# Optimization experiments

Hardware: AMD Instinct MI355X
Metric: run time of the kernel (lower is better)

## Reference

```python
import jax, jax.numpy as jnp
import numpy as np

B, N, C = 2, 65536, 256
HEADS, DIM_HEAD, SLICE_NUM = 8, 64, 64
INNER = HEADS * DIM_HEAD


def setup_inputs() -> dict:
    key = jax.random.key(0)
    ks = jax.random.split(key, 7)
    s_in = 1.0 / np.sqrt(C)
    s_dh = 1.0 / np.sqrt(DIM_HEAD)
    return {
        "x": jax.random.normal(ks[0], (B, N, C), dtype=jnp.float32),
        "Wx": jax.random.uniform(ks[1], (C, INNER), jnp.float32, -s_in, s_in),
        "bx": jax.random.uniform(ks[2], (INNER,), jnp.float32, -s_in, s_in),
        "Wfx": jax.random.uniform(ks[3], (C, INNER), jnp.float32, -s_in, s_in),
        "bfx": jax.random.uniform(ks[4], (INNER,), jnp.float32, -s_in, s_in),
        "Wslice": jax.random.uniform(ks[5], (DIM_HEAD, SLICE_NUM), jnp.float32, -s_dh, s_dh),
        "bslice": jax.random.uniform(ks[6], (SLICE_NUM,), jnp.float32, -s_dh, s_dh),
        "temperature": jnp.ones((1, HEADS, 1, 1), dtype=jnp.float32) * 0.5,
    }


def reference(x, Wx, bx, Wfx, bfx, Wslice, bslice, temperature):
    b, n, _ = x.shape
    # Linear projections, split heads: (B, N, H*D) -> (B, H, N, D)
    px = (x @ Wx + bx).reshape(b, n, HEADS, DIM_HEAD).transpose(0, 2, 1, 3)
    fx = (x @ Wfx + bfx).reshape(b, n, HEADS, DIM_HEAD).transpose(0, 2, 1, 3)
    # Project onto slices: (B, H, N, S)
    slice_proj = px @ Wslice + bslice
    # Temperature-scaled softmax over slices
    temp = jnp.clip(temperature, 0.5, 5.0)
    slice_weights = jax.nn.softmax(slice_proj / temp, axis=-1)
    # Normalize by per-slice mass over tokens, then aggregate
    slice_norm = slice_weights.sum(axis=2)  # (B, H, S)
    normed = slice_weights / (slice_norm[:, :, None, :] + 0.01)
    slice_tokens = jnp.einsum("bhns,bhnd->bhsd", normed, fx)
    return slice_tokens
```

## Files before the change

kernel.cpp:

```cpp
#include <hip/hip_runtime.h>
#include <hip/hip_bf16.h>


typedef __attribute__((ext_vector_type(8))) short short8;
typedef __attribute__((ext_vector_type(4))) short short4v;
typedef __attribute__((ext_vector_type(4))) float float4v;
typedef __attribute__((ext_vector_type(2))) unsigned int uint2v;

#define WPITCH 264
#define MP 36

__device__ __forceinline__ unsigned short f2bf(float f) {
    union { float f; unsigned int u; } v; v.f = f;
    unsigned int r = (v.u + 0x7FFFu + ((v.u >> 16) & 1u)) >> 16;
    return (unsigned short)r;
}

__device__ __forceinline__ unsigned int pack2(float a, float b) {
    __hip_bfloat162 h = __float22bfloat162_rn(float2{a, b});
    union { __hip_bfloat162 h; unsigned int u; } cv; cv.h = h;
    return cv.u;
}

__global__ __launch_bounds__(256)
void msfe_xprep(const float* __restrict__ x, unsigned short* __restrict__ xf) {
    __shared__ unsigned short Xs[64 * WPITCH];
    const int blk = blockIdx.x;
    const int tid = threadIdx.x;
    const float4v* xg = (const float4v*)(x + (long)blk * 64 * 256);
    #pragma unroll
    for (int i = 0; i < 16; ++i) {
        float4v v = xg[tid + i * 256];
        int f = (tid + i * 256) * 4;
        int row = f >> 8, col = f & 255;
        unsigned int lo = pack2(v.x, v.y), hi = pack2(v.z, v.w);
        *(unsigned int*)(Xs + row * WPITCH + col)     = lo;
        *(unsigned int*)(Xs + row * WPITCH + col + 2) = hi;
    }
    __syncthreads();
    const int wv = tid >> 6, lane = tid & 63;
    const int quad = lane >> 4, l16 = lane & 15;
    const int chunkL = wv >> 1, tw = wv & 1;
    unsigned short* ob = xf + (((long)(blk * 2 + chunkL) * 2 + tw) * 4096) + (long)lane * 8;
    const int row0 = chunkL * 32 + tw * 16 + l16;
    #pragma unroll
    for (int ks = 0; ks < 8; ++ks) {
        short8 o = *(const short8*)(Xs + row0 * WPITCH + ks * 32 + quad * 8);
        *(short8*)(ob + ks * 512) = o;
    }
}

__global__ __launch_bounds__(256)
void msfe_prep4(const float* __restrict__ Wx, const float* __restrict__ bx,
                const float* __restrict__ Wfx,
                const float* __restrict__ Wslice, const float* __restrict__ bslice,
                unsigned short* __restrict__ WtF, float* __restrict__ bcv) {
    const int b = blockIdx.x, t = threadIdx.x;
    if (b < 256) {
        const int head = b >> 5, oct = b & 31;
        __shared__ float Wsl[64 * 65];
        __shared__ float WxS[8 * 64];
        __shared__ unsigned short stg[8 * 64];
        #pragma unroll
        for (int i = 0; i < 16; ++i) {
            int idx = i * 256 + t; int d = idx >> 6, s = idx & 63;
            Wsl[d * 65 + s] = Wslice[idx];
        }
        #pragma unroll
        for (int i = 0; i < 2; ++i) {
            int idx = i * 256 + t; int j = idx >> 6, d = idx & 63;
            WxS[j * 64 + d] = Wx[(long)(oct * 8 + j) * 512 + head * 64 + d];
        }
        __syncthreads();
        const int s = t & 63;
        #pragma unroll
        for (int rep = 0; rep < 2; ++rep) {
            int j = (t >> 6) + rep * 4;
            float a0 = 0.f, a1 = 0.f, a2 = 0.f, a3 = 0.f;
            #pragma unroll
            for (int d = 0; d < 64; d += 4) {
                a0 += WxS[j * 64 + d]     * Wsl[(d)     * 65 + s];
                a1 += WxS[j * 64 + d + 1] * Wsl[(d + 1) * 65 + s];
                a2 += WxS[j * 64 + d + 2] * Wsl[(d + 2) * 65 + s];
                a3 += WxS[j * 64 + d + 3] * Wsl[(d + 3) * 65 + s];
            }
            stg[j * 64 + s] = f2bf((a0 + a1) + (a2 + a3));
        }
        __syncthreads();
        if (t < 64) {
            int nt = t >> 4, l16 = t & 15;
            int ks = oct >> 2, quad = oct & 3;
            int lane = quad * 16 + l16;
            short8 o;
            #pragma unroll
            for (int j = 0; j < 8; ++j) o[j] = (short)stg[j * 64 + nt * 16 + l16];
            *(short8*)(WtF + ((((long)(0 * 8 + head) * 4 + nt) * 8 + ks) * 64 + lane) * 8) = o;
        }
    } else if (b < 320) {
        const int head = (b - 256) >> 3, ks = (b - 256) & 7;
        const int nt = t >> 6, lane = t & 63;
        const int quad = lane >> 4, l16 = lane & 15;
        short8 o;
        #pragma unroll
        for (int j = 0; j < 8; ++j)
            o[j] = (short)f2bf(Wfx[(long)(ks * 32 + quad * 8 + j) * 512 + head * 64 + nt * 16 + l16]);
        *(short8*)(WtF + ((((long)(1 * 8 + head) * 4 + nt) * 8 + ks) * 64 + lane) * 8) = o;
    } else {
        #pragma unroll
        for (int p = 0; p < 2; ++p) {
            int j = t + p * 256;
            int h = j >> 6, s = j & 63;
            float bsum = bslice[s];
            for (int d = 0; d < 64; ++d) bsum += bx[h * 64 + d] * Wslice[d * 64 + s];
            bcv[j] = bsum;
        }
    }
}

__global__ __launch_bounds__(256, 2)
void msfe_main5(const unsigned short* __restrict__ xf,
                const unsigned short* __restrict__ WtF,
                const float* __restrict__ bcv,
                const float* __restrict__ bfx,
                const float* __restrict__ temperature,
                float* __restrict__ Tg, float* __restrict__ ng) {
    __shared__ unsigned short wT[2][64 * MP];
    __shared__ unsigned short fT[2][64 * MP];

    const int tid  = threadIdx.x;
    const int lane = tid & 63;
    const int wv   = tid >> 6;
    const int quad = lane >> 4;
    const int l16  = lane & 15;

    const int bidx = blockIdx.x;
    const int tile = (bidx >> 6) * 8 + (bidx & 7);
    const int head = (bidx >> 3) & 7;
    const int batch = tile >> 7;

    const int proj = wv >> 1;
    const int tw   = wv & 1;

    short8 wfr[4][8];
    {
        const unsigned short* wb = WtF + (((long)(proj * 8 + head) * 4) * 8) * 512 + (long)lane * 8;
        #pragma unroll
        for (int nt = 0; nt < 4; ++nt)
            #pragma unroll
            for (int ks = 0; ks < 8; ++ks)
                wfr[nt][ks] = *(const short8*)(wb + (nt * 8 + ks) * 512);
    }
    #pragma unroll
    for (int nt = 0; nt < 4; ++nt)
        #pragma unroll
        for (int ks = 0; ks < 8; ++ks)
            asm volatile("" : "+a"(wfr[nt][ks]));

    float bias[4];
    #pragma unroll
    for (int nt = 0; nt < 4; ++nt)
        bias[nt] = (proj == 0 ? bcv : bfx)[head * 64 + nt * 16 + l16];
    float tmp = temperature[head];
    tmp = fminf(fmaxf(tmp, 0.5f), 5.0f);
    const float invt = 1.0f / tmp;

    float4v Tac[4];
    #pragma unroll
    for (int nt = 0; nt < 4; ++nt) Tac[nt] = (float4v){0.f, 0.f, 0.f, 0.f};
    float normAcc[4] = {0.f, 0.f, 0.f, 0.f};

    const unsigned short* xb = xf + (((long)tile * 16 * 2 + tw) * 4096) + (long)lane * 8;
    short8 afr[8];
    #pragma unroll
    for (int ks = 0; ks < 8; ++ks)
        afr[ks] = *(const short8*)(xb + ks * 512);

    for (int c = 0; c < 16; ++c) {
        const int wbuf = c & 1, rbuf = wbuf ^ 1;

        float4v acc[4];
        #pragma unroll
        for (int nt = 0; nt < 4; ++nt) acc[nt] = (float4v){0.f, 0.f, 0.f, 0.f};
        #pragma unroll
        for (int ks = 0; ks < 8; ++ks) {
            #pragma unroll
            for (int nt = 0; nt < 4; ++nt)
                acc[nt] = __builtin_amdgcn_mfma_f32_16x16x32_bf16(afr[ks], wfr[nt][ks], acc[nt], 0, 0, 0);
        }

        if (c < 15) {
            #pragma unroll
            for (int ks = 0; ks < 8; ++ks)
                afr[ks] = *(const short8*)(xb + (long)(c + 1) * 8192 + ks * 512);
        }

        if (c > 0) {
            short8 a = *(const short8*)(&wT[rbuf][(wv * 16 + l16) * MP + quad * 8]);
            #pragma unroll
            for (int nt = 0; nt < 4; ++nt) {
                short8 bf = *(const short8*)(&fT[rbuf][(nt * 16 + l16) * MP + quad * 8]);
                Tac[nt] = __builtin_amdgcn_mfma_f32_16x16x32_bf16(a, bf, Tac[nt], 0, 0, 0);
            }
        }

        if (proj == 0) {
            float e[4][4];
            #pragma unroll
            for (int nt = 0; nt < 4; ++nt)
                #pragma unroll
                for (int rr = 0; rr < 4; ++rr)
                    e[nt][rr] = __expf((acc[nt][rr] + bias[nt]) * invt);
            #pragma unroll
            for (int rr = 0; rr < 4; ++rr) {
                float s = e[0][rr] + e[1][rr] + e[2][rr] + e[3][rr];
                s += __shfl_xor(s, 1); s += __shfl_xor(s, 2);
                s += __shfl_xor(s, 4); s += __shfl_xor(s, 8);
                float inv = 1.0f / s;
                e[0][rr] *= inv; e[1][rr] *= inv; e[2][rr] *= inv; e[3][rr] *= inv;
            }
            #pragma unroll
            for (int nt = 0; nt < 4; ++nt) {
                normAcc[nt] += e[nt][0] + e[nt][1] + e[nt][2] + e[nt][3];
                uint2v p;
                p.x = pack2(e[nt][0], e[nt][1]);
                p.y = pack2(e[nt][2], e[nt][3]);
                *(uint2v*)(&wT[wbuf][(nt * 16 + l16) * MP + tw * 16 + quad * 4]) = p;
            }
        } else {
            #pragma unroll
            for (int nt = 0; nt < 4; ++nt) {
                uint2v p;
                p.x = pack2(acc[nt][0] + bias[nt], acc[nt][1] + bias[nt]);
                p.y = pack2(acc[nt][2] + bias[nt], acc[nt][3] + bias[nt]);
                *(uint2v*)(&fT[wbuf][(nt * 16 + l16) * MP + tw * 16 + quad * 4]) = p;
            }
        }

        __syncthreads();
    }

    {
        short8 a = *(const short8*)(&wT[1][(wv * 16 + l16) * MP + quad * 8]);
        #pragma unroll
        for (int nt = 0; nt < 4; ++nt) {
            short8 bf = *(const short8*)(&fT[1][(nt * 16 + l16) * MP + quad * 8]);
            Tac[nt] = __builtin_amdgcn_mfma_f32_16x16x32_bf16(a, bf, Tac[nt], 0, 0, 0);
        }
    }

    const int basehs = (batch * 8 + head) * 64;
    #pragma unroll
    for (int nt = 0; nt < 4; ++nt) {
        #pragma unroll
        for (int rr = 0; rr < 4; ++rr) {
            int s = wv * 16 + quad * 4 + rr;
            int d = nt * 16 + l16;
            atomicAdd(&Tg[(basehs + s) * 64 + d], Tac[nt][rr]);
        }
    }
    if (proj == 0) {
        #pragma unroll
        for (int nt = 0; nt < 4; ++nt) {
            float v = normAcc[nt];
            v += __shfl_xor(v, 16);
            v += __shfl_xor(v, 32);
            if (quad == 0) atomicAdd(&ng[basehs + nt * 16 + l16], v);
        }
    }
}

__global__ void msfe_final(const float* __restrict__ Tg, const float* __restrict__ ng,
                           float* __restrict__ out) {
    int i = blockIdx.x * 256 + threadIdx.x;
    out[i] = Tg[i] / (ng[i >> 6] + 0.01f);
}

extern "C" void kernel_launch(void* const* d_in, const int* in_sizes, int n_in,
                              void* d_out, int out_size, void* d_ws, size_t ws_size,
                              hipStream_t stream) {
    const float* x       = (const float*)d_in[0];
    const float* Wx      = (const float*)d_in[1];
    const float* bx      = (const float*)d_in[2];
    const float* Wfx     = (const float*)d_in[3];
    const float* bfx     = (const float*)d_in[4];
    const float* Wslice  = (const float*)d_in[5];
    const float* bslice  = (const float*)d_in[6];
    const float* temp    = (const float*)d_in[7];

    char* ws = (char*)d_ws;
    unsigned short* xf  = (unsigned short*)ws;
    unsigned short* WtF = (unsigned short*)(ws + 67108864);
    float* bc = (float*)(ws + 67633152);
    float* Tg = (float*)(ws + 67635200);
    float* ng = (float*)(ws + 67897344);

    hipMemsetAsync(Tg, 0, 262144 + 4096, stream);
    msfe_prep4<<<321, 256, 0, stream>>>(Wx, bx, Wfx, Wslice, bslice, WtF, bc);
    msfe_xprep<<<2048, 256, 0, stream>>>(x, xf);
    msfe_main5<<<2048, 256, 0, stream>>>(xf, WtF, bc, bfx, temp, Tg, ng);
    msfe_final<<<256, 256, 0, stream>>>(Tg, ng, (float*)d_out);
}
```

Before: 337.4 us.

## Fuse x bf16 conversion into main kernel and fold temperature into exp2 bias

Removes the separate x-prep kernel that converted x to bf16 in an MFMA-friendly layout. The main kernel now loads fp32 x rows directly and packs them to bf16 in registers, which saves a full write and re-read of a 64MB intermediate. Each wave in the main kernel reads x, so four waves read the fp32 data (twice the bytes of the bf16 copy), with less coalesced row-strided loads. Separately, log2(e)/temperature is precomputed so the softmax uses exp2f with a single fma.

```diff
diff --git a/kernel.cpp b/kernel.cpp
--- a/kernel.cpp
+++ b/kernel.cpp
@@ -3,11 +3,9 @@
 
 
 typedef __attribute__((ext_vector_type(8))) short short8;
-typedef __attribute__((ext_vector_type(4))) short short4v;
 typedef __attribute__((ext_vector_type(4))) float float4v;
 typedef __attribute__((ext_vector_type(2))) unsigned int uint2v;
 
-#define WPITCH 264
 #define MP 36
 
 __device__ __forceinline__ unsigned short f2bf(float f) {
@@ -23,38 +21,12 @@
 }
 
 __global__ __launch_bounds__(256)
-void msfe_xprep(const float* __restrict__ x, unsigned short* __restrict__ xf) {
-    __shared__ unsigned short Xs[64 * WPITCH];
-    const int blk = blockIdx.x;
-    const int tid = threadIdx.x;
-    const float4v* xg = (const float4v*)(x + (long)blk * 64 * 256);
-    #pragma unroll
-    for (int i = 0; i < 16; ++i) {
-        float4v v = xg[tid + i * 256];
-        int f = (tid + i * 256) * 4;
-        int row = f >> 8, col = f & 255;
-        unsigned int lo = pack2(v.x, v.y), hi = pack2(v.z, v.w);
-        *(unsigned int*)(Xs + row * WPITCH + col)     = lo;
-        *(unsigned int*)(Xs + row * WPITCH + col + 2) = hi;
-    }
-    __syncthreads();
-    const int wv = tid >> 6, lane = tid & 63;
-    const int quad = lane >> 4, l16 = lane & 15;
-    const int chunkL = wv >> 1, tw = wv & 1;
-    unsigned short* ob = xf + (((long)(blk * 2 + chunkL) * 2 + tw) * 4096) + (long)lane * 8;
-    const int row0 = chunkL * 32 + tw * 16 + l16;
-    #pragma unroll
-    for (int ks = 0; ks < 8; ++ks) {
-        short8 o = *(const short8*)(Xs + row0 * WPITCH + ks * 32 + quad * 8);
-        *(short8*)(ob + ks * 512) = o;
-    }
-}
-
-__global__ __launch_bounds__(256)
-void msfe_prep4(const float* __restrict__ Wx, const float* __restrict__ bx,
+void msfe_prep5(const float* __restrict__ Wx, const float* __restrict__ bx,
                 const float* __restrict__ Wfx,
                 const float* __restrict__ Wslice, const float* __restrict__ bslice,
-                unsigned short* __restrict__ WtF, float* __restrict__ bcv) {
+                const float* __restrict__ temperature,
+                unsigned short* __restrict__ WtF, float* __restrict__ bcE,
+                float* __restrict__ kE) {
     const int b = blockIdx.x, t = threadIdx.x;
     if (b < 256) {
         const int head = b >> 5, oct = b & 31;
@@ -106,23 +78,29 @@
             o[j] = (short)f2bf(Wfx[(long)(ks * 32 + quad * 8 + j) * 512 + head * 64 + nt * 16 + l16]);
         *(short8*)(WtF + ((((long)(1 * 8 + head) * 4 + nt) * 8 + ks) * 64 + lane) * 8) = o;
     } else {
+        const float L2E = 1.4426950408889634f;
+        if (t < 8) {
+            float tv = fminf(fmaxf(temperature[t], 0.5f), 5.0f);
+            kE[t] = L2E / tv;
+        }
         #pragma unroll
         for (int p = 0; p < 2; ++p) {
             int j = t + p * 256;
             int h = j >> 6, s = j & 63;
             float bsum = bslice[s];
             for (int d = 0; d < 64; ++d) bsum += bx[h * 64 + d] * Wslice[d * 64 + s];
-            bcv[j] = bsum;
+            float tv = fminf(fmaxf(temperature[h], 0.5f), 5.0f);
+            bcE[j] = bsum * (L2E / tv);
         }
     }
 }
 
 __global__ __launch_bounds__(256, 2)
-void msfe_main5(const unsigned short* __restrict__ xf,
+void msfe_main6(const float* __restrict__ x,
                 const unsigned short* __restrict__ WtF,
-                const float* __restrict__ bcv,
+                const float* __restrict__ bcE,
                 const float* __restrict__ bfx,
-                const float* __restrict__ temperature,
+                const float* __restrict__ kE,
                 float* __restrict__ Tg, float* __restrict__ ng) {
     __shared__ unsigned short wT[2][64 * MP];
     __shared__ unsigned short fT[2][64 * MP];
@@ -159,21 +137,25 @@
     float bias[4];
     #pragma unroll
     for (int nt = 0; nt < 4; ++nt)
-        bias[nt] = (proj == 0 ? bcv : bfx)[head * 64 + nt * 16 + l16];
-    float tmp = temperature[head];
-    tmp = fminf(fmaxf(tmp, 0.5f), 5.0f);
-    const float invt = 1.0f / tmp;
+        bias[nt] = (proj == 0 ? bcE : bfx)[head * 64 + nt * 16 + l16];
+    const float kEh = kE[head];
 
     float4v Tac[4];
     #pragma unroll
     for (int nt = 0; nt < 4; ++nt) Tac[nt] = (float4v){0.f, 0.f, 0.f, 0.f};
     float normAcc[4] = {0.f, 0.f, 0.f, 0.f};
 
-    const unsigned short* xb = xf + (((long)tile * 16 * 2 + tw) * 4096) + (long)lane * 8;
+    const float* xrow = x + ((long)tile * 512 + tw * 16 + l16) * 256;
     short8 afr[8];
     #pragma unroll
-    for (int ks = 0; ks < 8; ++ks)
-        afr[ks] = *(const short8*)(xb + ks * 512);
+    for (int ks = 0; ks < 8; ++ks) {
+        const float4v* p = (const float4v*)(xrow + ks * 32 + quad * 8);
+        float4v v0 = p[0], v1 = p[1];
+        union { short8 s; unsigned int u[4]; } cu;
+        cu.u[0] = pack2(v0.x, v0.y); cu.u[1] = pack2(v0.z, v0.w);
+        cu.u[2] = pack2(v1.x, v1.y); cu.u[3] = pack2(v1.z, v1.w);
+        afr[ks] = cu.s;
+    }
 
     for (int c = 0; c < 16; ++c) {
         const int wbuf = c & 1, rbuf = wbuf ^ 1;
@@ -190,8 +172,14 @@
 
         if (c < 15) {
             #pragma unroll
-            for (int ks = 0; ks < 8; ++ks)
-                afr[ks] = *(const short8*)(xb + (long)(c + 1) * 8192 + ks * 512);
+            for (int ks = 0; ks < 8; ++ks) {
+                const float4v* p = (const float4v*)(xrow + (long)(c + 1) * 8192 + ks * 32 + quad * 8);
+                float4v v0 = p[0], v1 = p[1];
+                union { short8 s; unsigned int u[4]; } cu;
+                cu.u[0] = pack2(v0.x, v0.y); cu.u[1] = pack2(v0.z, v0.w);
+                cu.u[2] = pack2(v1.x, v1.y); cu.u[3] = pack2(v1.z, v1.w);
+                afr[ks] = cu.s;
+            }
         }
 
         if (c > 0) {
@@ -209,7 +197,7 @@
             for (int nt = 0; nt < 4; ++nt)
                 #pragma unroll
                 for (int rr = 0; rr < 4; ++rr)
-                    e[nt][rr] = __expf((acc[nt][rr] + bias[nt]) * invt);
+                    e[nt][rr] = exp2f(fmaf(acc[nt][rr], kEh, bias[nt]));
             #pragma unroll
             for (int rr = 0; rr < 4; ++rr) {
                 float s = e[0][rr] + e[1][rr] + e[2][rr] + e[3][rr];
@@ -288,15 +276,14 @@
     const float* temp    = (const float*)d_in[7];
 
     char* ws = (char*)d_ws;
-    unsigned short* xf  = (unsigned short*)ws;
-    unsigned short* WtF = (unsigned short*)(ws + 67108864);
-    float* bc = (float*)(ws + 67633152);
-    float* Tg = (float*)(ws + 67635200);
-    float* ng = (float*)(ws + 67897344);
+    unsigned short* WtF = (unsigned short*)ws;
+    float* bcE = (float*)(ws + 524288);
+    float* kE  = (float*)(ws + 526336);
+    float* Tg  = (float*)(ws + 528384);
+    float* ng  = (float*)(ws + 790528);
 
     hipMemsetAsync(Tg, 0, 262144 + 4096, stream);
-    msfe_prep4<<<321, 256, 0, stream>>>(Wx, bx, Wfx, Wslice, bslice, WtF, bc);
-    msfe_xprep<<<2048, 256, 0, stream>>>(x, xf);
-    msfe_main5<<<2048, 256, 0, stream>>>(xf, WtF, bc, bfx, temp, Tg, ng);
+    msfe_prep5<<<321, 256, 0, stream>>>(Wx, bx, Wfx, Wslice, bslice, temp, WtF, bcE, kE);
+    msfe_main6<<<2048, 256, 0, stream>>>(x, WtF, bcE, bfx, kE, Tg, ng);
     msfe_final<<<256, 256, 0, stream>>>(Tg, ng, (float*)d_out);
 }
```

New measurement: 555.6 us. 1.65x slower.
